# Kernel optimization log

Measured on AMD Instinct MI355X. Metric: run time of the kernel, lower is better.

The kernel has to match this reference:

```python
import jax, jax.numpy as jnp
import numpy as np

N_NODES = 524288
N_EDGES = 4194304
NUM_GRAPHS = 4096
F_IN = 4
PHI_HID = 128
PHI_OUT = 128
F_HID = 256
SCORE_DIM = 2


def _glorot(key, fan_in, fan_out):
    s = jnp.sqrt(2.0 / (fan_in + fan_out)).astype(jnp.float32)
    return jax.random.normal(key, (fan_in, fan_out), dtype=jnp.float32) * s


def setup_inputs() -> dict:
    key = jax.random.key(0)
    ks = jax.random.split(key, 16)
    x = jax.random.normal(ks[0], (N_NODES, F_IN), dtype=jnp.float32)
    edge_index = jax.random.randint(ks[1], (2, N_EDGES), 0, N_NODES, dtype=jnp.int64)
    batch = jnp.sort(jax.random.randint(ks[2], (N_NODES,), 0, NUM_GRAPHS, dtype=jnp.int64))
    # Phi MLP: in -> hid -> hid -> out (num_layers=2 hidden blocks)
    phi_w0 = _glorot(ks[3], F_IN, PHI_HID); phi_b0 = jnp.zeros((PHI_HID,), jnp.float32)
    phi_w1 = _glorot(ks[4], PHI_HID, PHI_HID); phi_b1 = jnp.zeros((PHI_HID,), jnp.float32)
    phi_w2 = _glorot(ks[5], PHI_HID, PHI_OUT); phi_b2 = jnp.zeros((PHI_OUT,), jnp.float32)
    # F MLP head: in -> hid -> hid -> score_dim
    f_w0 = _glorot(ks[6], PHI_OUT, F_HID); f_b0 = jnp.zeros((F_HID,), jnp.float32)
    f_w1 = _glorot(ks[7], F_HID, F_HID); f_b1 = jnp.zeros((F_HID,), jnp.float32)
    f_w2 = _glorot(ks[8], F_HID, SCORE_DIM); f_b2 = jnp.zeros((SCORE_DIM,), jnp.float32)
    return {"x": x, "edge_index": edge_index, "batch": batch,
            "phi_w0": phi_w0, "phi_b0": phi_b0, "phi_w1": phi_w1, "phi_b1": phi_b1,
            "phi_w2": phi_w2, "phi_b2": phi_b2,
            "f_w0": f_w0, "f_b0": f_b0, "f_w1": f_w1, "f_b1": f_b1,
            "f_w2": f_w2, "f_b2": f_b2}


def reference(x, edge_index, batch,
              phi_w0, phi_b0, phi_w1, phi_b1, phi_w2, phi_b2,
              f_w0, f_b0, f_w1, f_b1, f_w2, f_b2):
    # PhiMessagePassing.update ignores aggr_out: the scatter-add over edge_index
    # is mathematically dead. Node update = phi(x) per node.
    h = jax.nn.relu(x @ phi_w0 + phi_b0)          # [N, PHI_HID]
    h = jax.nn.relu(h @ phi_w1 + phi_b1)          # [N, PHI_HID]
    h = h @ phi_w2 + phi_b2                        # [N, PHI_OUT]
    # global_add_pool: segment sum by graph id
    g = jax.ops.segment_sum(h, batch, num_segments=NUM_GRAPHS)  # [G, PHI_OUT]
    # F head MLP
    g = jax.nn.relu(g @ f_w0 + f_b0)
    g = jax.nn.relu(g @ f_w1 + f_b1)
    out = g @ f_w2 + f_b2                          # [G, SCORE_DIM]
    return out
```

## Files before the change

### kernel.cpp

```cpp
#include <hip/hip_runtime.h>
#include <hip/hip_bf16.h>

#define NNODES   524288
#define NGRAPHS  4096
#define GS       12

typedef __attribute__((ext_vector_type(8)))  short short8;
typedef __attribute__((ext_vector_type(4)))  float f32x4;
typedef __attribute__((ext_vector_type(16))) float f32x16;

static __device__ __forceinline__ unsigned short f2bf(float f) {
    __hip_bfloat16 h = __float2bfloat16(f);
    return *reinterpret_cast<unsigned short*>(&h);
}

static __device__ __forceinline__ int swz(int node, int chunk) {
    return node * 128 + ((chunk ^ (node & 15)) << 3);
}

__global__ __launch_bounds__(256) void prep_weights(
        const float* __restrict__ w0, const float* __restrict__ w1,
        const float* __restrict__ w2,
        unsigned short* __restrict__ w0F, unsigned short* __restrict__ w1F,
        unsigned short* __restrict__ w2F, float* __restrict__ g) {
    const int e = blockIdx.x * 256 + threadIdx.x;
    reinterpret_cast<float4*>(g)[e] = make_float4(0.f, 0.f, 0.f, 0.f);
    if (e < 16384) {
        const int j = e & 7, lane = (e >> 3) & 63, ks = (e >> 9) & 7, q = (e >> 12) & 3;
        const int of = q * 32 + (lane & 31);
        const int k  = ks * 16 + (lane >> 5) * 8 + j;
        w1F[e] = f2bf(w1[k * 128 + of]);
    } else if (e < 32768) {
        const int i = e - 16384;
        const int j = i & 7, lane = (i >> 3) & 63, ks = (i >> 9) & 7, q = (i >> 12) & 3;
        const int of = q * 32 + (lane & 31);
        const int k  = ks * 16 + (lane >> 5) * 8 + j;
        w2F[i] = f2bf(w2[k * 128 + of]);
    } else if (e < 34816) {
        const int i = e - 32768;
        const int j = i & 7, lane = (i >> 3) & 63, q = (i >> 9) & 3;
        const int of = q * 32 + (lane & 31);
        const int k  = (lane >> 5) * 8 + j;
        w0F[i] = (k < 4) ? f2bf(w0[k * 128 + of]) : (unsigned short)0;
    }
}

__global__ __launch_bounds__(256, 4) void phi_kernel(
        const float* __restrict__ x, const int* __restrict__ batch,
        const unsigned short* __restrict__ w0F, const float* __restrict__ b0,
        const unsigned short* __restrict__ w1F, const float* __restrict__ b1,
        const unsigned short* __restrict__ w2F, const float* __restrict__ b2,
        float* __restrict__ g) {
    __shared__ __align__(16) unsigned short hb[2 * 64 * 128];
    unsigned short* const h1 = hb;
    unsigned short* const h2 = hb + 64 * 128;
    const int tid  = threadIdx.x;
    const int lane = tid & 63;
    const int q    = tid >> 6;
    const int n0   = blockIdx.x * 64;
    const int l31  = lane & 31;
    const int h    = lane >> 5;

    const int gi = batch[n0 + lane];
    const int gp = __shfl_up(gi, 1);
    const unsigned long long mask = __ballot((lane == 0) || (gi != gp));

    f32x16 acc[2];

    auto writeback = [&](const float* __restrict__ bias, unsigned short* __restrict__ dst) {
        #pragma unroll
        for (int g4 = 0; g4 < 4; ++g4) {
            const int of0 = q*32 + 8*g4 + 4*h;
            const float4 bv = *reinterpret_cast<const float4*>(bias + of0);
            #pragma unroll
            for (int nt = 0; nt < 2; ++nt) {
                const int node = nt*32 + l31;
                const f32x16 A = acc[nt];
                ushort4 s;
                s.x = f2bf(fmaxf(A[g4*4+0] + bv.x, 0.f));
                s.y = f2bf(fmaxf(A[g4*4+1] + bv.y, 0.f));
                s.z = f2bf(fmaxf(A[g4*4+2] + bv.z, 0.f));
                s.w = f2bf(fmaxf(A[g4*4+3] + bv.w, 0.f));
                *reinterpret_cast<ushort4*>(&dst[swz(node, q*4 + g4) + h*4]) = s;
            }
        }
    };

    {
        const short8 af = *reinterpret_cast<const short8*>(w0F + (q*64 + lane)*8);
        short8 bf[2];
        #pragma unroll
        for (int nt = 0; nt < 2; ++nt) {
            const float4 xv = *reinterpret_cast<const float4*>(
                x + (size_t)(n0 + nt*32 + l31) * 4);
            short8 v = (short8){0,0,0,0,0,0,0,0};
            if (h == 0) {
                v[0] = (short)f2bf(xv.x); v[1] = (short)f2bf(xv.y);
                v[2] = (short)f2bf(xv.z); v[3] = (short)f2bf(xv.w);
            }
            bf[nt] = v;
        }
        acc[0] = (f32x16){}; acc[1] = (f32x16){};
        #pragma unroll
        for (int nt = 0; nt < 2; ++nt)
            acc[nt] = __builtin_amdgcn_mfma_f32_32x32x16_bf16(
                af, bf[nt], acc[nt], 0, 0, 0);
    }
    writeback(b0, h1);
    __syncthreads();

    acc[0] = (f32x16){}; acc[1] = (f32x16){};
    #pragma unroll
    for (int ks = 0; ks < 8; ++ks) {
        const short8 a = *reinterpret_cast<const short8*>(
            w1F + ((q*8 + ks)*64 + lane)*8);
        short8 b[2];
        #pragma unroll
        for (int nt = 0; nt < 2; ++nt)
            b[nt] = *reinterpret_cast<const short8*>(
                &h1[swz(nt*32 + l31, ks*2 + h)]);
        #pragma unroll
        for (int nt = 0; nt < 2; ++nt)
            acc[nt] = __builtin_amdgcn_mfma_f32_32x32x16_bf16(
                a, b[nt], acc[nt], 0, 0, 0);
    }
    writeback(b1, h2);
    __syncthreads();

    acc[0] = (f32x16){}; acc[1] = (f32x16){};
    #pragma unroll
    for (int ks = 0; ks < 8; ++ks) {
        short8 a[2];
        #pragma unroll
        for (int mtn = 0; mtn < 2; ++mtn)
            a[mtn] = *reinterpret_cast<const short8*>(
                &h2[swz(mtn*32 + l31, ks*2 + h)]);
        const short8 bb = *reinterpret_cast<const short8*>(
            w2F + ((q*8 + ks)*64 + lane)*8);
        #pragma unroll
        for (int mtn = 0; mtn < 2; ++mtn)
            acc[mtn] = __builtin_amdgcn_mfma_f32_32x32x16_bf16(
                a[mtn], bb, acc[mtn], 0, 0, 0);
    }

    const float b2v = b2[q*32 + l31];

    if (mask == 1ull) {
        float val = 0.f;
        #pragma unroll
        for (int mtn = 0; mtn < 2; ++mtn) {
            const f32x16 A = acc[mtn];
            #pragma unroll
            for (int r = 0; r < 16; ++r) val += A[r];
        }
        val += __shfl_xor(val, 32);
        if (h == 0)
            atomicAdd(g + (size_t)gi * 128 + q*32 + l31, fmaf(64.f, b2v, val));
    } else {
        unsigned long long rem = mask & (mask - 1);
        int s = 0;
        while (true) {
            const int e = rem ? (int)__builtin_ctzll(rem) : 64;
            const int grun = __shfl(gi, s);
            const float cnt = (float)(e - s);
            float val = 0.f;
            #pragma unroll
            for (int mtn = 0; mtn < 2; ++mtn) {
                const f32x16 A = acc[mtn];
                #pragma unroll
                for (int r = 0; r < 16; ++r) {
                    const int node = mtn*32 + (r & 3) + 8*(r >> 2) + 4*h;
                    const float inc = (node >= s && node < e) ? 1.f : 0.f;
                    val = fmaf(A[r], inc, val);
                }
            }
            val += __shfl_xor(val, 32);
            if (h == 0)
                atomicAdd(g + (size_t)grun * 128 + q*32 + l31, fmaf(cnt, b2v, val));
            if (!rem) break;
            s = e;
            rem &= rem - 1;
        }
    }
}

__global__ __launch_bounds__(256) void head_kernel(
        const float* __restrict__ g,
        const float* __restrict__ fw0, const float* __restrict__ fb0,
        const float* __restrict__ fw1, const float* __restrict__ fb1,
        const float* __restrict__ fw2, const float* __restrict__ fb2,
        float* __restrict__ out) {
    __shared__ float gS[128 * GS];
    __shared__ float h1T[256 * GS];
    __shared__ float red[4][8];
    const int tid = threadIdx.x;
    const int g0  = blockIdx.x * 4;

    {
        const int gr = tid >> 6, k0 = (tid & 63) * 2;
        const float2 v = *reinterpret_cast<const float2*>(
            g + (size_t)(g0 + gr) * 128 + k0);
        gS[(k0+0)*GS + gr] = v.x;
        gS[(k0+1)*GS + gr] = v.y;
    }
    __syncthreads();

    float a1[4];
    #pragma unroll
    for (int i = 0; i < 4; ++i) a1[i] = 0.f;
    #pragma unroll 4
    for (int k = 0; k < 128; ++k) {
        const float w = fw0[k * 256 + tid];
        const f32x4 v0 = *reinterpret_cast<const f32x4*>(&gS[k*GS]);
        #pragma unroll
        for (int j = 0; j < 4; ++j)
            a1[j] = fmaf(v0[j], w, a1[j]);
    }
    {
        const float bb = fb0[tid];
        f32x4 s0;
        #pragma unroll
        for (int j = 0; j < 4; ++j)
            s0[j] = fmaxf(a1[j] + bb, 0.f);
        *reinterpret_cast<f32x4*>(&h1T[tid*GS]) = s0;
    }
    __syncthreads();

    float a2[4];
    #pragma unroll
    for (int i = 0; i < 4; ++i) a2[i] = 0.f;
    #pragma unroll 4
    for (int k = 0; k < 256; ++k) {
        const float w = fw1[k * 256 + tid];
        const f32x4 v0 = *reinterpret_cast<const f32x4*>(&h1T[k*GS]);
        #pragma unroll
        for (int j = 0; j < 4; ++j)
            a2[j] = fmaf(v0[j], w, a2[j]);
    }

    float p[8];
    {
        const float bb  = fb1[tid];
        const float w2a = fw2[tid*2 + 0];
        const float w2b = fw2[tid*2 + 1];
        #pragma unroll
        for (int i = 0; i < 4; ++i) {
            const float h2 = fmaxf(a2[i] + bb, 0.f);
            p[i*2 + 0] = h2 * w2a;
            p[i*2 + 1] = h2 * w2b;
        }
    }
    #pragma unroll
    for (int i = 0; i < 8; ++i) {
        float v = p[i];
        v += __shfl_xor(v, 32); v += __shfl_xor(v, 16); v += __shfl_xor(v, 8);
        v += __shfl_xor(v, 4);  v += __shfl_xor(v, 2);  v += __shfl_xor(v, 1);
        p[i] = v;
    }
    if ((tid & 63) == 0) {
        #pragma unroll
        for (int i = 0; i < 8; ++i) red[tid >> 6][i] = p[i];
    }
    __syncthreads();
    if (tid < 8)
        out[g0*2 + tid] = red[0][tid] + red[1][tid] + red[2][tid] + red[3][tid]
                        + fb2[tid & 1];
}

extern "C" void kernel_launch(void* const* d_in, const int* in_sizes, int n_in,
                              void* d_out, int out_size, void* d_ws, size_t ws_size,
                              hipStream_t stream) {
    const float* x   = (const float*)d_in[0];
    const int*   batch = (const int*)d_in[2];
    const float* w0  = (const float*)d_in[3];
    const float* b0  = (const float*)d_in[4];
    const float* w1  = (const float*)d_in[5];
    const float* b1  = (const float*)d_in[6];
    const float* w2  = (const float*)d_in[7];
    const float* b2  = (const float*)d_in[8];
    const float* fw0 = (const float*)d_in[9];
    const float* fb0 = (const float*)d_in[10];
    const float* fw1 = (const float*)d_in[11];
    const float* fb1 = (const float*)d_in[12];
    const float* fw2 = (const float*)d_in[13];
    const float* fb2 = (const float*)d_in[14];
    float* out = (float*)d_out;

    float* g = (float*)d_ws;
    unsigned short* w1F = (unsigned short*)((char*)d_ws + (size_t)NGRAPHS * 128 * 4);
    unsigned short* w2F = w1F + 128 * 128;
    unsigned short* w0F = w2F + 128 * 128;

    prep_weights<<<512, 256, 0, stream>>>(w0, w1, w2, w0F, w1F, w2F, g);
    phi_kernel<<<NNODES / 64, 256, 0, stream>>>(x, batch, w0F, b0, w1F, b1, w2F, b2, g);
    head_kernel<<<NGRAPHS / 4, 256, 0, stream>>>(g, fw0, fb0, fw1, fb1, fw2, fb2, out);
}
```

Baseline: 179.0 us.

## Fold phi's final linear layer into head's first layer via linearity of pooling

Because segment_sum is linear, the last phi layer (w2,b2) is pooled-then-applied instead of applied per node. Its product with the head's first weight is precomputed in prep_weights, and per-graph node counts are accumulated to carry the folded bias. This removes one 128x128 per-node matmul and one LDS staging buffer from phi_kernel, and occupancy hint is raised from 4 to 6. It adds a small fp32 weight-product precompute, with some prep threads each doing 128-long dot products, plus extra per-run count atomics.

Result: faster. 168.8 us (-5.7%).

```diff
diff --git a/kernel.cpp b/kernel.cpp
--- a/kernel.cpp
+++ b/kernel.cpp
@@ -20,40 +20,49 @@
 
 __global__ __launch_bounds__(256) void prep_weights(
         const float* __restrict__ w0, const float* __restrict__ w1,
-        const float* __restrict__ w2,
+        const float* __restrict__ w2, const float* __restrict__ fw0,
+        const float* __restrict__ b2,
         unsigned short* __restrict__ w0F, unsigned short* __restrict__ w1F,
-        unsigned short* __restrict__ w2F, float* __restrict__ g) {
+        float* __restrict__ W0p, float* __restrict__ c0p,
+        float* __restrict__ Pz) {
     const int e = blockIdx.x * 256 + threadIdx.x;
-    reinterpret_cast<float4*>(g)[e] = make_float4(0.f, 0.f, 0.f, 0.f);
+    if (e < 132096)
+        reinterpret_cast<float4*>(Pz)[e] = make_float4(0.f, 0.f, 0.f, 0.f);
     if (e < 16384) {
         const int j = e & 7, lane = (e >> 3) & 63, ks = (e >> 9) & 7, q = (e >> 12) & 3;
         const int of = q * 32 + (lane & 31);
         const int k  = ks * 16 + (lane >> 5) * 8 + j;
         w1F[e] = f2bf(w1[k * 128 + of]);
-    } else if (e < 32768) {
+    } else if (e < 18432) {
         const int i = e - 16384;
-        const int j = i & 7, lane = (i >> 3) & 63, ks = (i >> 9) & 7, q = (i >> 12) & 3;
-        const int of = q * 32 + (lane & 31);
-        const int k  = ks * 16 + (lane >> 5) * 8 + j;
-        w2F[i] = f2bf(w2[k * 128 + of]);
-    } else if (e < 34816) {
-        const int i = e - 32768;
         const int j = i & 7, lane = (i >> 3) & 63, q = (i >> 9) & 3;
         const int of = q * 32 + (lane & 31);
         const int k  = (lane >> 5) * 8 + j;
         w0F[i] = (k < 4) ? f2bf(w0[k * 128 + of]) : (unsigned short)0;
-    }
-}
-
-__global__ __launch_bounds__(256, 4) void phi_kernel(
+    } else if (e < 51200) {
+        const int i = e - 18432;
+        const int o = i & 255, kp = i >> 8;
+        float v = 0.f;
+        #pragma unroll 8
+        for (int of = 0; of < 128; ++of)
+            v = fmaf(w2[kp * 128 + of], fw0[of * 256 + o], v);
+        W0p[kp * 256 + o] = v;
+    } else if (e < 51456) {
+        const int o = e - 51200;
+        float v = 0.f;
+        #pragma unroll 8
+        for (int of = 0; of < 128; ++of)
+            v = fmaf(b2[of], fw0[of * 256 + o], v);
+        c0p[o] = v;
+    }
+}
+
+__global__ __launch_bounds__(256, 6) void phi_kernel(
         const float* __restrict__ x, const int* __restrict__ batch,
         const unsigned short* __restrict__ w0F, const float* __restrict__ b0,
         const unsigned short* __restrict__ w1F, const float* __restrict__ b1,
-        const unsigned short* __restrict__ w2F, const float* __restrict__ b2,
-        float* __restrict__ g) {
-    __shared__ __align__(16) unsigned short hb[2 * 64 * 128];
-    unsigned short* const h1 = hb;
-    unsigned short* const h2 = hb + 64 * 128;
+        float* __restrict__ P, float* __restrict__ cnts) {
+    __shared__ __align__(16) unsigned short h1[64 * 128];
     const int tid  = threadIdx.x;
     const int lane = tid & 63;
     const int q    = tid >> 6;
@@ -66,25 +75,6 @@
     const unsigned long long mask = __ballot((lane == 0) || (gi != gp));
 
     f32x16 acc[2];
-
-    auto writeback = [&](const float* __restrict__ bias, unsigned short* __restrict__ dst) {
-        #pragma unroll
-        for (int g4 = 0; g4 < 4; ++g4) {
-            const int of0 = q*32 + 8*g4 + 4*h;
-            const float4 bv = *reinterpret_cast<const float4*>(bias + of0);
-            #pragma unroll
-            for (int nt = 0; nt < 2; ++nt) {
-                const int node = nt*32 + l31;
-                const f32x16 A = acc[nt];
-                ushort4 s;
-                s.x = f2bf(fmaxf(A[g4*4+0] + bv.x, 0.f));
-                s.y = f2bf(fmaxf(A[g4*4+1] + bv.y, 0.f));
-                s.z = f2bf(fmaxf(A[g4*4+2] + bv.z, 0.f));
-                s.w = f2bf(fmaxf(A[g4*4+3] + bv.w, 0.f));
-                *reinterpret_cast<ushort4*>(&dst[swz(node, q*4 + g4) + h*4]) = s;
-            }
-        }
-    };
 
     {
         const short8 af = *reinterpret_cast<const short8*>(w0F + (q*64 + lane)*8);
@@ -106,25 +96,22 @@
             acc[nt] = __builtin_amdgcn_mfma_f32_32x32x16_bf16(
                 af, bf[nt], acc[nt], 0, 0, 0);
     }
-    writeback(b0, h1);
-    __syncthreads();
-
-    acc[0] = (f32x16){}; acc[1] = (f32x16){};
-    #pragma unroll
-    for (int ks = 0; ks < 8; ++ks) {
-        const short8 a = *reinterpret_cast<const short8*>(
-            w1F + ((q*8 + ks)*64 + lane)*8);
-        short8 b[2];
-        #pragma unroll
-        for (int nt = 0; nt < 2; ++nt)
-            b[nt] = *reinterpret_cast<const short8*>(
-                &h1[swz(nt*32 + l31, ks*2 + h)]);
-        #pragma unroll
-        for (int nt = 0; nt < 2; ++nt)
-            acc[nt] = __builtin_amdgcn_mfma_f32_32x32x16_bf16(
-                a, b[nt], acc[nt], 0, 0, 0);
-    }
-    writeback(b1, h2);
+    #pragma unroll
+    for (int g4 = 0; g4 < 4; ++g4) {
+        const int of0 = q*32 + 8*g4 + 4*h;
+        const float4 bv = *reinterpret_cast<const float4*>(b0 + of0);
+        #pragma unroll
+        for (int nt = 0; nt < 2; ++nt) {
+            const int node = nt*32 + l31;
+            const f32x16 A = acc[nt];
+            ushort4 s;
+            s.x = f2bf(fmaxf(A[g4*4+0] + bv.x, 0.f));
+            s.y = f2bf(fmaxf(A[g4*4+1] + bv.y, 0.f));
+            s.z = f2bf(fmaxf(A[g4*4+2] + bv.z, 0.f));
+            s.w = f2bf(fmaxf(A[g4*4+3] + bv.w, 0.f));
+            *reinterpret_cast<ushort4*>(&h1[swz(node, q*4 + g4) + h*4]) = s;
+        }
+    }
     __syncthreads();
 
     acc[0] = (f32x16){}; acc[1] = (f32x16){};
@@ -134,16 +121,21 @@
         #pragma unroll
         for (int mtn = 0; mtn < 2; ++mtn)
             a[mtn] = *reinterpret_cast<const short8*>(
-                &h2[swz(mtn*32 + l31, ks*2 + h)]);
+                &h1[swz(mtn*32 + l31, ks*2 + h)]);
         const short8 bb = *reinterpret_cast<const short8*>(
-            w2F + ((q*8 + ks)*64 + lane)*8);
+            w1F + ((q*8 + ks)*64 + lane)*8);
         #pragma unroll
         for (int mtn = 0; mtn < 2; ++mtn)
             acc[mtn] = __builtin_amdgcn_mfma_f32_32x32x16_bf16(
                 a[mtn], bb, acc[mtn], 0, 0, 0);
     }
 
-    const float b2v = b2[q*32 + l31];
+    const float b1v = b1[q*32 + l31];
+    #pragma unroll
+    for (int mtn = 0; mtn < 2; ++mtn)
+        #pragma unroll
+        for (int r = 0; r < 16; ++r)
+            acc[mtn][r] = fmaxf(acc[mtn][r] + b1v, 0.f);
 
     if (mask == 1ull) {
         float val = 0.f;
@@ -155,14 +147,15 @@
         }
         val += __shfl_xor(val, 32);
         if (h == 0)
-            atomicAdd(g + (size_t)gi * 128 + q*32 + l31, fmaf(64.f, b2v, val));
+            atomicAdd(P + (size_t)gi * 128 + q*32 + l31, val);
+        if (tid == 0)
+            atomicAdd(cnts + gi, 64.f);
     } else {
         unsigned long long rem = mask & (mask - 1);
         int s = 0;
         while (true) {
             const int e = rem ? (int)__builtin_ctzll(rem) : 64;
             const int grun = __shfl(gi, s);
-            const float cnt = (float)(e - s);
             float val = 0.f;
             #pragma unroll
             for (int mtn = 0; mtn < 2; ++mtn) {
@@ -176,7 +169,9 @@
             }
             val += __shfl_xor(val, 32);
             if (h == 0)
-                atomicAdd(g + (size_t)grun * 128 + q*32 + l31, fmaf(cnt, b2v, val));
+                atomicAdd(P + (size_t)grun * 128 + q*32 + l31, val);
+            if (tid == 0)
+                atomicAdd(cnts + grun, (float)(e - s));
             if (!rem) break;
             s = e;
             rem &= rem - 1;
@@ -185,21 +180,24 @@
 }
 
 __global__ __launch_bounds__(256) void head_kernel(
-        const float* __restrict__ g,
-        const float* __restrict__ fw0, const float* __restrict__ fb0,
+        const float* __restrict__ P, const float* __restrict__ cnts,
+        const float* __restrict__ W0p, const float* __restrict__ c0p,
+        const float* __restrict__ fb0,
         const float* __restrict__ fw1, const float* __restrict__ fb1,
         const float* __restrict__ fw2, const float* __restrict__ fb2,
         float* __restrict__ out) {
     __shared__ float gS[128 * GS];
     __shared__ float h1T[256 * GS];
     __shared__ float red[4][8];
+    __shared__ float cntS[4];
     const int tid = threadIdx.x;
     const int g0  = blockIdx.x * 4;
 
+    if (tid < 4) cntS[tid] = cnts[g0 + tid];
     {
         const int gr = tid >> 6, k0 = (tid & 63) * 2;
         const float2 v = *reinterpret_cast<const float2*>(
-            g + (size_t)(g0 + gr) * 128 + k0);
+            P + (size_t)(g0 + gr) * 128 + k0);
         gS[(k0+0)*GS + gr] = v.x;
         gS[(k0+1)*GS + gr] = v.y;
     }
@@ -210,7 +208,7 @@
     for (int i = 0; i < 4; ++i) a1[i] = 0.f;
     #pragma unroll 4
     for (int k = 0; k < 128; ++k) {
-        const float w = fw0[k * 256 + tid];
+        const float w = W0p[k * 256 + tid];
         const f32x4 v0 = *reinterpret_cast<const f32x4*>(&gS[k*GS]);
         #pragma unroll
         for (int j = 0; j < 4; ++j)
@@ -218,10 +216,11 @@
     }
     {
         const float bb = fb0[tid];
+        const float cc = c0p[tid];
         f32x4 s0;
         #pragma unroll
         for (int j = 0; j < 4; ++j)
-            s0[j] = fmaxf(a1[j] + bb, 0.f);
+            s0[j] = fmaxf(fmaf(cntS[j], cc, a1[j]) + bb, 0.f);
         *reinterpret_cast<f32x4*>(&h1T[tid*GS]) = s0;
     }
     __syncthreads();
@@ -286,12 +285,15 @@
     const float* fb2 = (const float*)d_in[14];
     float* out = (float*)d_out;
 
-    float* g = (float*)d_ws;
-    unsigned short* w1F = (unsigned short*)((char*)d_ws + (size_t)NGRAPHS * 128 * 4);
-    unsigned short* w2F = w1F + 128 * 128;
-    unsigned short* w0F = w2F + 128 * 128;
-
-    prep_weights<<<512, 256, 0, stream>>>(w0, w1, w2, w0F, w1F, w2F, g);
-    phi_kernel<<<NNODES / 64, 256, 0, stream>>>(x, batch, w0F, b0, w1F, b1, w2F, b2, g);
-    head_kernel<<<NGRAPHS / 4, 256, 0, stream>>>(g, fw0, fb0, fw1, fb1, fw2, fb2, out);
-}
+    float* P    = (float*)d_ws;
+    float* cnts = P + (size_t)NGRAPHS * 128;
+    unsigned short* w1F = (unsigned short*)(cnts + NGRAPHS);
+    unsigned short* w0F = w1F + 16384;
+    float* W0p = (float*)(w0F + 2048);
+    float* c0p = W0p + 128 * 256;
+
+    prep_weights<<<516, 256, 0, stream>>>(w0, w1, w2, fw0, b2, w0F, w1F, W0p, c0p, P);
+    phi_kernel<<<NNODES / 64, 256, 0, stream>>>(x, batch, w0F, b0, w1F, b1, P, cnts);
+    head_kernel<<<NGRAPHS / 4, 256, 0, stream>>>(P, cnts, W0p, c0p, fb0,
+                                                 fw1, fb1, fw2, fb2, out);
+}
```
